# Kernel tuning notes

Measured on AMD Instinct MI355X. Metric: run time of the kernel, lower is better.

## Reference

```python
import jax, jax.numpy as jnp
import numpy as np

N_EMBD = 256; N_HEAD = 16; CTX = 2048
V_HD = 32; KV_RANK = 32; Q_RANK = 96
ROPE_HD = 64; NOPE_HD = 32; HEAD_D = ROPE_HD + NOPE_HD  # 96
N_KEEP = CTX // 4  # 512
C_CURV = 1.0
EPS = 1e-6
B, T = 2, 2048


def rmsnorm(x, w):
    return x * jax.lax.rsqrt(jnp.mean(x * x, axis=-1, keepdims=True) + EPS) * w


def logmap(x, u, c):
    # log map from hyperbolic point x toward u (Poincare ball, curvature c)
    xn = jnp.linalg.norm(x, axis=-1, keepdims=True)
    sf = 2.0 / (1.0 + c * xn ** 2)                      # scaling_factor(x, c)
    mx = -x
    un = jnp.linalg.norm(u, axis=-1, keepdims=True)
    ip = jnp.sum(mx * u, axis=-1, keepdims=True)
    num = (1 + 2 * c * ip + c * un ** 2) * mx + (1 - c * xn ** 2) * u
    den = 1 + 2 * c * ip + (c ** 2) * (xn ** 2) * (un ** 2)
    mob = num / den                                      # mobius_addition(-x, u, c)
    an = jnp.linalg.norm(mob, axis=-1, keepdims=True)
    cf = 2.0 / (sf * (c ** 0.5))
    arg = jnp.clip(jnp.sqrt(c) * jnp.sqrt(an), -0.999, 0.999)
    return cf * jnp.arctanh(arg) * (mob / an)


def rope_apply(x, cos_seq, sin_seq):
    # x: [B,H,T,D]; cos/sin: [T,D//2] -> broadcast [1,1,T,D//2]
    c = cos_seq[None, None]; s = sin_seq[None, None]
    xr, xi = jnp.split(x, 2, axis=-1)
    return jnp.concatenate([xr * c - xi * s, xr * s + xi * c], axis=-1)


def attn(q, k, v, causal):
    d = q.shape[-1]
    s = jnp.einsum('bhqd,bhkd->bhqk', q, k) / jnp.sqrt(jnp.asarray(d, q.dtype))
    if causal:
        mask = jnp.tril(jnp.ones((s.shape[-2], s.shape[-1]), bool))
        s = jnp.where(mask, s, -jnp.inf)
    p = jax.nn.softmax(s, axis=-1)
    return jnp.einsum('bhqk,bhkd->bhqd', p, v)


def setup_inputs() -> dict:
    key = jax.random.key(0)
    ks = jax.random.split(key, 20)
    w = lambda k, shp: (jax.random.normal(k, shp, jnp.float32) * 0.02)
    NOPE_DIM = N_HEAD * NOPE_HD   # 512
    ROPE_DIM = N_HEAD * ROPE_HD   # 1024
    VAL_DIM = N_HEAD * V_HD       # 512
    # precompute_freqs_cis(rope_head_dim, ctx_len)
    freqs = 1.0 / (10000.0 ** (np.arange(0, ROPE_HD, 2, dtype=np.float32) / ROPE_HD))
    t = np.arange(CTX, dtype=np.float32)
    ang = np.outer(t, freqs)
    return {
        'x': jax.random.normal(ks[0], (B, T, N_EMBD), jnp.float32),
        'W_cq': w(ks[1], (N_EMBD, Q_RANK)),
        'q_norm_w': jnp.ones((Q_RANK,), jnp.float32),
        'W_dqn': w(ks[2], (Q_RANK, NOPE_DIM)),
        'W_dqr': w(ks[3], (Q_RANK, ROPE_DIM)),
        'W_ckv': w(ks[4], (N_EMBD, KV_RANK)),
        'kv_norm_w': jnp.ones((KV_RANK,), jnp.float32),
        'W_dkn': w(ks[5], (KV_RANK, NOPE_DIM)),
        'W_dv': w(ks[6], (KV_RANK, VAL_DIM)),
        'W_kr': w(ks[7], (N_EMBD, ROPE_HD)),
        'W_imp': w(ks[8], (N_EMBD, 1)),
        'b_imp': jnp.zeros((1,), jnp.float32),
        'W_selk': w(ks[9], (N_EMBD, N_HEAD * HEAD_D)),
        'W_selv': w(ks[10], (N_EMBD, VAL_DIM)),
        'W_wink': w(ks[11], (N_EMBD, N_HEAD * HEAD_D)),
        'W_winv': w(ks[12], (N_EMBD, VAL_DIM)),
        'W_gate': w(ks[13], (N_EMBD, 3)),
        'b_gate': jnp.zeros((3,), jnp.float32),
        'W_proj': w(ks[14], (N_HEAD * V_HD, N_EMBD)),
        'cos_f': jnp.asarray(np.cos(ang)),
        'sin_f': jnp.asarray(np.sin(ang)),
    }


def reference(x, W_cq, q_norm_w, W_dqn, W_dqr, W_ckv, kv_norm_w, W_dkn, W_dv, W_kr,
              W_imp, b_imp, W_selk, W_selv, W_wink, W_winv, W_gate, b_gate, W_proj,
              cos_f, sin_f):
    Bx, Tx, C = x.shape
    ref = jnp.pad(x[:, :-1, :], ((0, 0), (1, 0), (0, 0)))   # calculate_reference_point
    xh = logmap(ref, x, C_CURV)
    # compressed query path
    nq = rmsnorm(xh @ W_cq, q_norm_w)
    qn = (nq @ W_dqn).reshape(Bx, Tx, N_HEAD, NOPE_HD).transpose(0, 2, 1, 3)
    qr = (nq @ W_dqr).reshape(Bx, Tx, N_HEAD, ROPE_HD).transpose(0, 2, 1, 3)
    qr = rope_apply(qr, cos_f[:Tx], sin_f[:Tx])
    q = jnp.concatenate([qn, qr], axis=-1)                  # [B,H,T,96]
    # branch gate
    bw = jax.nn.softmax(jnp.mean(x @ W_gate + b_gate, axis=1), axis=-1)  # [B,3]
    # compressed KV path
    nkv = rmsnorm(x @ W_ckv, kv_norm_w)
    kn = (nkv @ W_dkn).reshape(Bx, Tx, N_HEAD, NOPE_HD).transpose(0, 2, 1, 3)
    v = (nkv @ W_dv).reshape(Bx, Tx, N_HEAD, V_HD).transpose(0, 2, 1, 3)
    kr = rope_apply((x @ W_kr)[:, None], cos_f[:Tx], sin_f[:Tx])  # [B,1,T,64]
    kr = jnp.broadcast_to(kr, (Bx, N_HEAD, Tx, ROPE_HD))
    k = jnp.concatenate([kn, kr], axis=-1)
    out_cmp = attn(q, k, v, causal=True)
    # token-selection branch (top-k important tokens, sorted)
    scores = (x @ W_imp + b_imp)[..., 0]                    # [B,T]
    _, idx = jax.lax.top_k(scores, min(N_KEEP, Tx))
    idx = jnp.sort(idx, axis=1)
    sel = jnp.take_along_axis(x, idx[:, :, None], axis=1)   # [B,K,C]
    sk = (sel @ W_selk).reshape(Bx, -1, N_HEAD, HEAD_D).transpose(0, 2, 1, 3)
    sv = (sel @ W_selv).reshape(Bx, -1, N_HEAD, V_HD).transpose(0, 2, 1, 3)
    out_sel = attn(q, sk, sv, causal=False)
    # sliding-window branch (training path -> full sequence, causal)
    wk = (x @ W_wink).reshape(Bx, Tx, N_HEAD, HEAD_D).transpose(0, 2, 1, 3)
    wv = (x @ W_winv).reshape(Bx, Tx, N_HEAD, V_HD).transpose(0, 2, 1, 3)
    out_win = attn(q, wk, wv, causal=True)
    w3 = bw[:, :, None, None, None]
    out = w3[:, 0] * out_cmp + w3[:, 1] * out_sel + w3[:, 2] * out_win
    out = out.transpose(0, 2, 1, 3).reshape(Bx, Tx, N_HEAD * V_HD)
    return out @ W_proj
```

## Files before the change

### kernel.cpp

```cpp
#include <hip/hip_runtime.h>
#include <hip/hip_bf16.h>
#include <math.h>

#define TT 2048
#define NE 256
#define NHEAD 16

typedef __attribute__((ext_vector_type(8))) short bf16x8;
typedef __attribute__((ext_vector_type(4))) float f32x4;
typedef __attribute__((ext_vector_type(16))) float f32x16;
typedef unsigned short ushort;
typedef __attribute__((ext_vector_type(8))) unsigned short us8;

__device__ __forceinline__ short f2bf(float x) {
  __hip_bfloat16 h = __float2bfloat16(x);
  return *reinterpret_cast<short*>(&h);
}
__device__ __forceinline__ float bf2f(ushort u) {
  unsigned v = ((unsigned)u) << 16;
  return __uint_as_float(v);
}

__global__ __launch_bounds__(256) void logmap_kernel(const float* __restrict__ x,
                                                     ushort* __restrict__ xhb,
                                                     ushort* __restrict__ xbf) {
  __shared__ float red[16];
  int row = blockIdx.x, tid = threadIdx.x;
  int t = row & (TT - 1);
  float uv = x[row * NE + tid];
  float rv = (t == 0) ? 0.f : x[row * NE - NE + tid];
  xbf[row * NE + tid] = (ushort)f2bf(uv);
  float a = rv * rv, bq = uv * uv, c2 = -rv * uv;
#pragma unroll
  for (int off = 32; off > 0; off >>= 1) {
    a += __shfl_down(a, off, 64);
    bq += __shfl_down(bq, off, 64);
    c2 += __shfl_down(c2, off, 64);
  }
  if ((tid & 63) == 0) {
    int w = tid >> 6;
    red[w] = a; red[4 + w] = bq; red[8 + w] = c2;
  }
  __syncthreads();
  float xn2 = red[0] + red[1] + red[2] + red[3];
  float un2 = red[4] + red[5] + red[6] + red[7];
  float ip  = red[8] + red[9] + red[10] + red[11];
  float den = 1.f + 2.f * ip + xn2 * un2;
  float mob = ((1.f + 2.f * ip + un2) * (-rv) + (1.f - xn2) * uv) / den;
  float m2 = mob * mob;
#pragma unroll
  for (int off = 32; off > 0; off >>= 1) m2 += __shfl_down(m2, off, 64);
  if ((tid & 63) == 0) red[12 + (tid >> 6)] = m2;
  __syncthreads();
  float an2 = red[12] + red[13] + red[14] + red[15];
  float an = sqrtf(an2);
  float cf = 1.f + xn2;
  float arg = fminf(sqrtf(an), 0.999f);
  xhb[row * NE + tid] = (ushort)f2bf(cf * atanhf(arg) * mob / an);
}

__global__ __launch_bounds__(256) void wtconv_all_kernel(
    const float* __restrict__ W_dqn, const float* __restrict__ W_dqr,
    const float* __restrict__ W_dkn, const float* __restrict__ W_dv,
    const float* __restrict__ W_selk, const float* __restrict__ W_selv,
    const float* __restrict__ W_wink, const float* __restrict__ W_winv,
    const float* __restrict__ W_proj, const float* __restrict__ W_cq,
    const float* __restrict__ W_ckv, const float* __restrict__ W_kr,
    const float* __restrict__ W_gate, const float* __restrict__ W_imp,
    ushort* __restrict__ Wt_q, ushort* __restrict__ Wt_kv,
    ushort* __restrict__ Wt_sel, ushort* __restrict__ Wt_win,
    ushort* __restrict__ Wt_proj, ushort* __restrict__ Wt_cq,
    ushort* __restrict__ Wt_nkv) {
  int i = blockIdx.x * 256 + threadIdx.x;
  const float scale = 0.147244458176154f;
  if (i < 147456) {
    int k = i / 1536, n = i - k * 1536;
    float v = (n < 512) ? W_dqn[(size_t)k * 512 + n] : W_dqr[(size_t)k * 1024 + (n - 512)];
    Wt_q[(size_t)n * 96 + k] = (ushort)f2bf(v * scale);
  } else if (i < 180224) {
    int j = i - 147456;
    int k = j >> 10, n = j & 1023;
    float v = (n < 512) ? W_dkn[(size_t)k * 512 + n] : W_dv[(size_t)k * 512 + (n - 512)];
    Wt_kv[(size_t)n * 32 + k] = (ushort)f2bf(v);
  } else if (i < 704512) {
    int j = i - 180224;
    int k = j >> 11, n = j & 2047;
    float v = (n < 1536) ? W_selk[(size_t)k * 1536 + n] : W_selv[(size_t)k * 512 + (n - 1536)];
    Wt_sel[(size_t)n * 256 + k] = (ushort)f2bf(v);
  } else if (i < 1228800) {
    int j = i - 704512;
    int k = j >> 11, n = j & 2047;
    float v = (n < 1536) ? W_wink[(size_t)k * 1536 + n] : W_winv[(size_t)k * 512 + (n - 1536)];
    Wt_win[(size_t)n * 256 + k] = (ushort)f2bf(v);
  } else if (i < 1359872) {
    int j = i - 1228800;
    int k = j >> 8, n = j & 255;
    Wt_proj[(size_t)n * 512 + k] = (ushort)f2bf(W_proj[(size_t)k * 256 + n]);
  } else if (i < 1392640) {
    int j = i - 1359872;
    int k = j >> 7, n = j & 127;
    float v = (n < 96) ? W_cq[(size_t)k * 96 + n] : 0.f;
    Wt_cq[(size_t)n * 256 + k] = (ushort)f2bf(v);
  } else if (i < 1425408) {
    int j = i - 1392640;
    int k = j >> 7, n = j & 127;
    float v;
    if (n < 32) v = W_ckv[(size_t)k * 32 + n];
    else if (n < 96) v = W_kr[(size_t)k * 64 + (n - 32)];
    else if (n < 99) v = W_gate[(size_t)k * 3 + (n - 96)];
    else if (n == 99) v = W_imp[k];
    else v = 0.f;
    Wt_nkv[(size_t)n * 256 + k] = (ushort)f2bf(v);
  }
}

__global__ __launch_bounds__(256) void gemm_kernel(const ushort* __restrict__ A,
                                                   const ushort* __restrict__ Bt,
                                                   void* __restrict__ Out,
                                                   const ushort* __restrict__ A2,
                                                   const ushort* __restrict__ Bt2,
                                                   void* __restrict__ Out2,
                                                   const int* __restrict__ selidx,
                                                   const float* __restrict__ cosp,
                                                   const float* __restrict__ sinp,
                                                   int K, int ldo, int obf16, int ropemode) {
  __shared__ __align__(16) short As[128 * 40];
  __shared__ __align__(16) short Bs[128 * 40];
  if (blockIdx.z == 1) { A = A2; Bt = Bt2; Out = Out2; }
  int m0 = blockIdx.x * 128, n0 = blockIdx.y * 128;
  int tid = threadIdx.x;
  int wv = tid >> 6, lane = tid & 63;
  int l15 = lane & 15, quad = lane >> 4;
  int wm = wv >> 1, wn = wv & 1;

  int r = tid >> 1, seg = tid & 1;
  int arow = m0 + r;
  if (selidx) arow = ((arow >> 9) * TT) + selidx[m0 + r];
  const ushort* ga = A + (size_t)arow * K + seg * 16;
  const ushort* gb = Bt + (size_t)(n0 + r) * K + seg * 16;

  f32x4 acc[4][4];
#pragma unroll
  for (int i = 0; i < 4; ++i)
#pragma unroll
    for (int j = 0; j < 4; ++j) acc[i][j] = (f32x4){0.f, 0.f, 0.f, 0.f};

  int nk = K >> 5;
  us8 apre0 = *(const us8*)ga, apre1 = *(const us8*)(ga + 8);
  us8 bpre0 = *(const us8*)gb, bpre1 = *(const us8*)(gb + 8);
  for (int kk = 0; kk < nk; ++kk) {
    __syncthreads();
    *(us8*)(As + r * 40 + seg * 16) = apre0;
    *(us8*)(As + r * 40 + seg * 16 + 8) = apre1;
    *(us8*)(Bs + r * 40 + seg * 16) = bpre0;
    *(us8*)(Bs + r * 40 + seg * 16 + 8) = bpre1;
    __syncthreads();
    if (kk + 1 < nk) {
      apre0 = *(const us8*)(ga + (kk + 1) * 32);
      apre1 = *(const us8*)(ga + (kk + 1) * 32 + 8);
      bpre0 = *(const us8*)(gb + (kk + 1) * 32);
      bpre1 = *(const us8*)(gb + (kk + 1) * 32 + 8);
    }
    bf16x8 af[4], bf[4];
#pragma unroll
    for (int mf = 0; mf < 4; ++mf)
      af[mf] = *(const bf16x8*)(As + (wm * 64 + mf * 16 + l15) * 40 + quad * 8);
#pragma unroll
    for (int nf = 0; nf < 4; ++nf)
      bf[nf] = *(const bf16x8*)(Bs + (wn * 64 + nf * 16 + l15) * 40 + quad * 8);
#pragma unroll
    for (int mf = 0; mf < 4; ++mf)
#pragma unroll
      for (int nf = 0; nf < 4; ++nf)
        acc[mf][nf] = __builtin_amdgcn_mfma_f32_16x16x32_bf16(af[mf], bf[nf], acc[mf][nf], 0, 0, 0);
  }

  if (ropemode && blockIdx.y >= 4) {
#pragma unroll
    for (int mf = 0; mf < 4; ++mf) {
#pragma unroll
      for (int nf = 0; nf < 2; ++nf) {
        int dd = nf * 16 + l15;
#pragma unroll
        for (int reg = 0; reg < 4; ++reg) {
          int row = m0 + wm * 64 + mf * 16 + quad * 4 + reg;
          int t = row & (TT - 1);
          float c = cosp[t * 32 + dd], s = sinp[t * 32 + dd];
          float xr = acc[mf][nf][reg], xi = acc[mf][nf + 2][reg];
          int col = n0 + wn * 64 + nf * 16 + l15;
          size_t oi = (size_t)row * ldo + col;
          ((ushort*)Out)[oi] = (ushort)f2bf(xr * c - xi * s);
          ((ushort*)Out)[oi + 32] = (ushort)f2bf(xr * s + xi * c);
        }
      }
    }
    return;
  }
#pragma unroll
  for (int mf = 0; mf < 4; ++mf) {
#pragma unroll
    for (int nf = 0; nf < 4; ++nf) {
#pragma unroll
      for (int reg = 0; reg < 4; ++reg) {
        int row = m0 + wm * 64 + mf * 16 + quad * 4 + reg;
        int col = n0 + wn * 64 + nf * 16 + l15;
        size_t oi = (size_t)row * ldo + col;
        float v = acc[mf][nf][reg];
        if (obf16) ((ushort*)Out)[oi] = (ushort)f2bf(v);
        else ((float*)Out)[oi] = v;
      }
    }
  }
}

__global__ __launch_bounds__(128) void norm_kernel(const float* __restrict__ nkvraw,
                                                   const float* __restrict__ nqraw,
                                                   const float* __restrict__ x,
                                                   const float* __restrict__ W_imp,
                                                   const float* __restrict__ b_imp,
                                                   const float* __restrict__ kvnw,
                                                   const float* __restrict__ qnw,
                                                   const float* __restrict__ cos_t,
                                                   const float* __restrict__ sin_t,
                                                   ushort* __restrict__ nkvb,
                                                   ushort* __restrict__ krbf,
                                                   float* __restrict__ scores,
                                                   ushort* __restrict__ nqb) {
  int tid = threadIdx.x;
  if (blockIdx.x < 4096) {
    int row = blockIdx.x;
    int t = row & (TT - 1);
    if (tid < 32) {
      float v = nkvraw[(size_t)row * 128 + tid];
      float ss = v * v;
#pragma unroll
      for (int off = 16; off > 0; off >>= 1) ss += __shfl_xor(ss, off, 32);
      nkvb[(size_t)row * 32 + tid] = (ushort)f2bf(v * rsqrtf(ss / 32.f + 1e-6f) * kvnw[tid]);
    } else if (tid < 64) {
      int dd = tid - 32;
      float xr = nkvraw[(size_t)row * 128 + 32 + dd];
      float xi = nkvraw[(size_t)row * 128 + 64 + dd];
      float c = cos_t[t * 32 + dd], s = sin_t[t * 32 + dd];
      krbf[(size_t)row * 64 + dd] = (ushort)f2bf(xr * c - xi * s);
      krbf[(size_t)row * 64 + dd + 32] = (ushort)f2bf(xr * s + xi * c);
    } else {
      int lane = tid - 64;
      float p = 0.f;
#pragma unroll
      for (int k = 0; k < 4; ++k) p += x[(size_t)row * 256 + lane + k * 64] * W_imp[lane + k * 64];
#pragma unroll
      for (int off = 32; off > 0; off >>= 1) p += __shfl_down(p, off, 64);
      if (lane == 0) scores[row] = p + b_imp[0];
    }
  } else {
    int row = blockIdx.x - 4096;
    __shared__ float red2[2];
    float v = (tid < 96) ? nqraw[(size_t)row * 128 + tid] : 0.f;
    float p = v * v;
#pragma unroll
    for (int off = 32; off > 0; off >>= 1) p += __shfl_down(p, off, 64);
    if ((tid & 63) == 0) red2[tid >> 6] = p;
    __syncthreads();
    float ss = red2[0] + red2[1];
    float sc = rsqrtf(ss / 96.f + 1e-6f);
    if (tid < 96) nqb[(size_t)row * 96 + tid] = (ushort)f2bf(v * sc * qnw[tid]);
  }
}

__global__ __launch_bounds__(256) void gate_kernel(const float* __restrict__ nkvraw,
                                                   const float* __restrict__ b_gate,
                                                   float* __restrict__ bw) {
  int tid = threadIdx.x;
  float a0 = 0, a1 = 0, a2 = 0, a3 = 0, a4 = 0, a5 = 0;
  for (int r = tid; r < 2 * TT; r += 256) {
    float g0 = nkvraw[(size_t)r * 128 + 96];
    float g1 = nkvraw[(size_t)r * 128 + 97];
    float g2 = nkvraw[(size_t)r * 128 + 98];
    if (r < TT) { a0 += g0; a1 += g1; a2 += g2; }
    else { a3 += g0; a4 += g1; a5 += g2; }
  }
  __shared__ float red[6][256];
  red[0][tid] = a0; red[1][tid] = a1; red[2][tid] = a2;
  red[3][tid] = a3; red[4][tid] = a4; red[5][tid] = a5;
  __syncthreads();
  for (int s = 128; s > 0; s >>= 1) {
    if (tid < s) {
#pragma unroll
      for (int q = 0; q < 6; ++q) red[q][tid] += red[q][tid + s];
    }
    __syncthreads();
  }
  if (tid == 0) {
    for (int b = 0; b < 2; ++b) {
      float v[3];
      float mx = -INFINITY;
      for (int j = 0; j < 3; ++j) {
        v[j] = red[b * 3 + j][0] / (float)TT + b_gate[j];
        mx = fmaxf(mx, v[j]);
      }
      float sum = 0.f;
      for (int j = 0; j < 3; ++j) { v[j] = expf(v[j] - mx); sum += v[j]; }
      for (int j = 0; j < 3; ++j) bw[b * 3 + j] = v[j] / sum;
    }
  }
}

__global__ __launch_bounds__(1024) void topk_rank_kernel(const float* __restrict__ scores,
                                                         int* __restrict__ flags) {
  int b = blockIdx.y, blk = blockIdx.x;
  int tid = threadIdx.x;
  __shared__ unsigned sk[TT];
#pragma unroll
  for (int e = 0; e < 2; ++e) {
    int i = tid + e * 1024;
    float s = scores[b * TT + i];
    unsigned u = __float_as_uint(s);
    u = (u & 0x80000000u) ? ~u : (u | 0x80000000u);
    sk[i] = u;
  }
  __syncthreads();
  int e = blk * 64 + (tid >> 4);
  int sub = tid & 15;
  unsigned u = sk[e];
  int r = 0;
  int j0 = sub * 128;
#pragma unroll 8
  for (int j = j0; j < j0 + 128; ++j) {
    unsigned v = sk[j];
    r += (int)((v > u) || (v == u && j < e));
  }
#pragma unroll
  for (int off = 8; off > 0; off >>= 1) r += __shfl_down(r, off, 16);
  if (sub == 0) flags[b * TT + e] = (r < 512) ? 1 : 0;
}

__global__ __launch_bounds__(1024) void topk_scan_kernel(const int* __restrict__ flags,
                                                         int* __restrict__ selidx) {
  int b = blockIdx.x, tid = threadIdx.x;
  __shared__ int pre[TT];
  int f0 = flags[b * TT + tid], f1 = flags[b * TT + tid + 1024];
  pre[tid] = f0;
  pre[tid + 1024] = f1;
  __syncthreads();
  for (int off = 1; off < TT; off <<= 1) {
    int a0 = (tid >= off) ? pre[tid - off] : 0;
    int a1 = (tid + 1024 >= off) ? pre[tid + 1024 - off] : 0;
    __syncthreads();
    pre[tid] += a0;
    pre[tid + 1024] += a1;
    __syncthreads();
  }
  if (f0) selidx[b * 512 + pre[tid] - 1] = tid;
  if (f1) selidx[b * 512 + pre[tid + 1024] - 1] = tid + 1024;
}

__global__ __launch_bounds__(256, 2) void flash_fused_kernel(
    const ushort* __restrict__ qbf,
    const ushort* __restrict__ kv,
    const ushort* __restrict__ krbf,
    const ushort* __restrict__ selt,
    const ushort* __restrict__ wint,
    const float* __restrict__ bw,
    ushort* __restrict__ attout) {
  __shared__ __align__(16) short Qs[128 * 104];
  __shared__ __align__(16) short Ks[2][64 * 104];
  __shared__ __align__(16) short Vts[2][32 * 72];
  __shared__ float Ls[4][32];

  int bx = blockIdx.x;
  int j = bx >> 5;
  int qtile = (j < 8) ? (15 - 2 * j) : (2 * (j - 8));
  int bh = bx & 31;
  int b = bh >> 4, h = bh & 15;
  int tid = threadIdx.x;
  int wv = tid >> 6, lane = tid & 63;
  int l31 = lane & 31, half = lane >> 5;

  int qrow0 = qtile * 128;
  for (int i = tid; i < 128 * 24; i += 256) {
    int qi = i / 24, dp = (i - qi * 24) * 4;
    int col = (dp < 32) ? (h * 32 + dp) : (512 + h * 64 + (dp - 32));
    *(ushort4*)(Qs + qi * 104 + dp) =
        *(const ushort4*)(qbf + (size_t)(b * TT + qrow0 + qi) * 1536 + col);
  }
  __syncthreads();
  bf16x8 qf[6];
#pragma unroll
  for (int ks = 0; ks < 6; ++ks)
    qf[ks] = *(const bf16x8*)(Qs + (wv * 32 + l31) * 104 + ks * 16 + half * 8);

  short* kdst[6];
#pragma unroll
  for (int c = 0; c < 6; ++c) {
    int i = c * 256 + tid;
    int kj = i / 24, dp = (i - kj * 24) * 4;
    kdst[c] = &Ks[0][kj * 104 + dp];
  }
  short* vdsta[2];
  short* vdstb[2];
#pragma unroll
  for (int c = 0; c < 2; ++c) {
    int i = c * 256 + tid;
    int d0 = (i & 15) * 2, kjp = (i >> 4) * 2;
    vdsta[c] = &Vts[0][(d0 + 0) * 72 + kjp];
    vdstb[c] = &Vts[0][(d0 + 1) * 72 + kjp];
  }

  f32x16 oacc;
#pragma unroll
  for (int r = 0; r < 16; ++r) oacc[r] = 0.f;

  for (int s = 0; s < 3; ++s) {
    const ushort *kb1, *kb2, *vb;
    size_t krs1, krs2, vrs;
    int split, Tk, causal;
    if (s == 0) {
      kb1 = kv + h * 32;        krs1 = 1024; split = 32;
      kb2 = krbf;               krs2 = 64;
      vb = kv + 512 + h * 32;   vrs = 1024;
      Tk = TT; causal = 1;
    } else if (s == 1) {
      kb1 = selt + h * 96;      krs1 = 2048; split = 96;
      kb2 = selt;               krs2 = 2048;
      vb = selt + 1536 + h * 32; vrs = 2048;
      Tk = 512; causal = 0;
    } else {
      kb1 = wint + h * 96;      krs1 = 2048; split = 96;
      kb2 = wint;               krs2 = 2048;
      vb = wint + 1536 + h * 32; vrs = 2048;
      Tk = TT; causal = 1;
    }
    size_t bTk = (size_t)b * Tk;

    const ushort* ksrc[6];
    int kstep[6];
#pragma unroll
    for (int c = 0; c < 6; ++c) {
      int i = c * 256 + tid;
      int kj = i / 24, dp = (i - kj * 24) * 4;
      if (dp < split) { ksrc[c] = kb1 + (bTk + kj) * krs1 + dp; kstep[c] = (int)(64 * krs1); }
      else            { ksrc[c] = kb2 + (bTk + kj) * krs2 + (dp - split); kstep[c] = (int)(64 * krs2); }
    }
    const ushort* vsrcA[2];
    const ushort* vsrcB[2];
    int vstep = (int)(64 * vrs);
#pragma unroll
    for (int c = 0; c < 2; ++c) {
      int i = c * 256 + tid;
      int d0 = (i & 15) * 2, kjp = (i >> 4) * 2;
      vsrcA[c] = vb + (bTk + kjp) * vrs + d0;
      vsrcB[c] = vb + (bTk + kjp + 1) * vrs + d0;
    }

    ushort4 kpre0[6], kpre1[6];
    ushort2 vpa0[2], vpb0[2], vpa1[2], vpb1[2];

#define PREFETCH(KP, VA, VB)                                  \
  {                                                           \
    _Pragma("unroll") for (int c = 0; c < 6; ++c) {           \
      KP[c] = *(const ushort4*)ksrc[c];                       \
      ksrc[c] += kstep[c];                                    \
    }                                                         \
    _Pragma("unroll") for (int c = 0; c < 2; ++c) {           \
      VA[c] = *(const ushort2*)vsrcA[c];                      \
      VB[c] = *(const ushort2*)vsrcB[c];                      \
      vsrcA[c] += vstep;                                      \
      vsrcB[c] += vstep;                                      \
    }                                                         \
  }

#define COMMIT(KP, VA, VB, SL)                                           \
  {                                                                      \
    _Pragma("unroll") for (int c = 0; c < 6; ++c)                        \
      *(ushort4*)(kdst[c] + (SL) * (64 * 104)) = KP[c];                  \
    _Pragma("unroll") for (int c = 0; c < 2; ++c) {                      \
      *(unsigned*)(vdsta[c] + (SL) * (32 * 72)) =                        \
          (unsigned)VA[c].x | ((unsigned)VB[c].x << 16);                 \
      *(unsigned*)(vdstb[c] + (SL) * (32 * 72)) =                        \
          (unsigned)VA[c].y | ((unsigned)VB[c].y << 16);                 \
    }                                                                    \
  }

    f32x16 of;
#pragma unroll
    for (int r = 0; r < 16; ++r) of[r] = 0.f;
    float lsum = 0.f;

    auto do_tile = [&](int kt, const short* Kss, const short* Vss) {
      int krow0 = kt * 64;
      f32x16 sfT[2];
#pragma unroll
      for (int r = 0; r < 16; ++r) { sfT[0][r] = 0.f; sfT[1][r] = 0.f; }
#pragma unroll
      for (int ks = 0; ks < 6; ++ks) {
#pragma unroll
        for (int kb = 0; kb < 2; ++kb) {
          bf16x8 ak = *(const bf16x8*)(Kss + (kb * 32 + l31) * 104 + ks * 16 + half * 8);
          sfT[kb] = __builtin_amdgcn_mfma_f32_32x32x16_bf16(ak, qf[ks], sfT[kb], 0, 0, 0);
        }
      }
      int qg = qrow0 + wv * 32 + l31;
      int domask = causal && (kt >= 2 * qtile);
      unsigned w01[2][4], w23[2][4];
#pragma unroll
      for (int kb = 0; kb < 2; ++kb) {
#pragma unroll
        for (int g = 0; g < 4; ++g) {
          int key0 = krow0 + kb * 32 + 8 * g + 4 * half;
          float s0 = sfT[kb][g * 4 + 0];
          float s1 = sfT[kb][g * 4 + 1];
          float s2 = sfT[kb][g * 4 + 2];
          float s3 = sfT[kb][g * 4 + 3];
          if (domask) {
            if (key0 + 0 > qg) s0 = -INFINITY;
            if (key0 + 1 > qg) s1 = -INFINITY;
            if (key0 + 2 > qg) s2 = -INFINITY;
            if (key0 + 3 > qg) s3 = -INFINITY;
          }
          float p0 = __builtin_amdgcn_exp2f(fminf(s0, 43.3f));
          float p1 = __builtin_amdgcn_exp2f(fminf(s1, 43.3f));
          float p2 = __builtin_amdgcn_exp2f(fminf(s2, 43.3f));
          float p3 = __builtin_amdgcn_exp2f(fminf(s3, 43.3f));
          lsum += (p0 + p1) + (p2 + p3);
          asm("v_cvt_pk_bf16_f32 %0, %1, %2" : "=v"(w01[kb][g]) : "v"(p0), "v"(p1));
          asm("v_cvt_pk_bf16_f32 %0, %1, %2" : "=v"(w23[kb][g]) : "v"(p2), "v"(p3));
        }
      }
#pragma unroll
      for (int ks2 = 0; ks2 < 4; ++ks2) {
        int kb = ks2 >> 1, gA = 2 * (ks2 & 1);
        unsigned a0 = w01[kb][gA], b0 = w01[kb][gA + 1];
        unsigned a1 = w23[kb][gA], b1 = w23[kb][gA + 1];
        asm("v_permlane32_swap_b32 %0, %1" : "+v"(a0), "+v"(b0));
        asm("v_permlane32_swap_b32 %0, %1" : "+v"(a1), "+v"(b1));
        union { unsigned u[4]; bf16x8 v; } ap;
        ap.u[0] = a0; ap.u[1] = a1; ap.u[2] = b0; ap.u[3] = b1;
        bf16x8 bv = *(const bf16x8*)(Vss + l31 * 72 + ks2 * 16 + half * 8);
        of = __builtin_amdgcn_mfma_f32_32x32x16_bf16(ap.v, bv, of, 0, 0, 0);
      }
    };

    int nkt = causal ? (2 * qtile + 2) : 8;
    PREFETCH(kpre0, vpa0, vpb0);
    PREFETCH(kpre1, vpa1, vpb1);
    for (int kt = 0; kt < nkt; kt += 2) {
      COMMIT(kpre0, vpa0, vpb0, 0);
      if (kt + 2 < nkt) PREFETCH(kpre0, vpa0, vpb0);
      __syncthreads();
      do_tile(kt, Ks[0], Vts[0]);
      COMMIT(kpre1, vpa1, vpb1, 1);
      if (kt + 3 < nkt) PREFETCH(kpre1, vpa1, vpb1);
      __syncthreads();
      do_tile(kt + 1, Ks[1], Vts[1]);
    }
#undef PREFETCH
#undef COMMIT

    lsum += __shfl_xor(lsum, 32, 64);
    if (half == 0) Ls[wv][l31] = lsum;
    asm volatile("s_waitcnt lgkmcnt(0)" ::: "memory");
    float wgt = bw[b * 3 + s];
#pragma unroll
    for (int reg = 0; reg < 16; ++reg) {
      int ql = (reg & 3) + 8 * (reg >> 2) + 4 * half;
      oacc[reg] += of[reg] * (wgt / Ls[wv][ql]);
    }
  }

#pragma unroll
  for (int reg = 0; reg < 16; ++reg) {
    int trow = qrow0 + wv * 32 + (reg & 3) + 8 * (reg >> 2) + 4 * half;
    attout[(size_t)(b * TT + trow) * 512 + h * 32 + l31] = (ushort)f2bf(oacc[reg]);
  }
}

extern "C" void kernel_launch(void* const* d_in, const int* in_sizes, int n_in,
                              void* d_out, int out_size, void* d_ws, size_t ws_size,
                              hipStream_t stream) {
  const float* x      = (const float*)d_in[0];
  const float* W_cq   = (const float*)d_in[1];
  const float* qnw    = (const float*)d_in[2];
  const float* W_dqn  = (const float*)d_in[3];
  const float* W_dqr  = (const float*)d_in[4];
  const float* W_ckv  = (const float*)d_in[5];
  const float* kvnw   = (const float*)d_in[6];
  const float* W_dkn  = (const float*)d_in[7];
  const float* W_dv   = (const float*)d_in[8];
  const float* W_kr   = (const float*)d_in[9];
  const float* W_imp  = (const float*)d_in[10];
  const float* b_imp  = (const float*)d_in[11];
  const float* W_selk = (const float*)d_in[12];
  const float* W_selv = (const float*)d_in[13];
  const float* W_wink = (const float*)d_in[14];
  const float* W_winv = (const float*)d_in[15];
  const float* W_gate = (const float*)d_in[16];
  const float* b_gate = (const float*)d_in[17];
  const float* W_proj = (const float*)d_in[18];
  const float* cos_f  = (const float*)d_in[19];
  const float* sin_f  = (const float*)d_in[20];
  float* out = (float*)d_out;
  float* ws  = (float*)d_ws;

  size_t off = 0;
  auto alloc = [&](size_t n) {
    float* p = ws + off;
    off += (n + 255) & ~(size_t)255;
    return p;
  };
  const int ROWS = 2 * TT;
  ushort* xbf     = (ushort*)alloc((size_t)ROWS * 128);
  ushort* xhb     = (ushort*)alloc((size_t)ROWS * 128);
  float* nqraw    = alloc((size_t)ROWS * 128);
  float* nkvraw   = alloc((size_t)ROWS * 128);
  ushort* nqb     = (ushort*)alloc((size_t)ROWS * 48);
  ushort* qbf     = (ushort*)alloc((size_t)ROWS * 768);
  ushort* nkvb    = (ushort*)alloc((size_t)ROWS * 16);
  ushort* kvtmp   = (ushort*)alloc((size_t)ROWS * 512);
  ushort* krbf    = (ushort*)alloc((size_t)ROWS * 32);
  float* scores   = alloc(ROWS);
  float* bwp      = alloc(8);
  int* selidx     = (int*)alloc(1024);
  int* selflags   = (int*)alloc(ROWS);
  ushort* seltmp  = (ushort*)alloc((size_t)1024 * 1024);
  ushort* wintmp  = (ushort*)alloc((size_t)ROWS * 1024);
  ushort* attoutb = (ushort*)alloc((size_t)ROWS * 256);
  ushort* Wt_q    = (ushort*)alloc((size_t)1536 * 48);
  ushort* Wt_kv   = (ushort*)alloc((size_t)1024 * 16);
  ushort* Wt_sel  = (ushort*)alloc((size_t)2048 * 128);
  ushort* Wt_win  = (ushort*)alloc((size_t)2048 * 128);
  ushort* Wt_proj = (ushort*)alloc((size_t)256 * 256);
  ushort* Wt_cq   = (ushort*)alloc((size_t)128 * 128);
  ushort* Wt_nkv  = (ushort*)alloc((size_t)128 * 128);

  wtconv_all_kernel<<<5568, 256, 0, stream>>>(
      W_dqn, W_dqr, W_dkn, W_dv, W_selk, W_selv, W_wink, W_winv, W_proj,
      W_cq, W_ckv, W_kr, W_gate, W_imp,
      Wt_q, Wt_kv, Wt_sel, Wt_win, Wt_proj, Wt_cq, Wt_nkv);

  logmap_kernel<<<ROWS, 256, 0, stream>>>(x, xhb, xbf);

  gemm_kernel<<<dim3(32, 1, 2), 256, 0, stream>>>(xhb, Wt_cq, nqraw, xbf, Wt_nkv, nkvraw,
                                                  nullptr, nullptr, nullptr, 256, 128, 0, 0);
  norm_kernel<<<2 * ROWS, 128, 0, stream>>>(nkvraw, nqraw, x, W_imp, b_imp, kvnw, qnw,
                                            cos_f, sin_f, nkvb, krbf, scores, nqb);
  gemm_kernel<<<dim3(32, 12), 256, 0, stream>>>(nqb, Wt_q, qbf, nullptr, nullptr, nullptr,
                                                nullptr, cos_f, sin_f, 96, 1536, 1, 1);
  gemm_kernel<<<dim3(32, 8), 256, 0, stream>>>(nkvb, Wt_kv, kvtmp, nullptr, nullptr, nullptr,
                                               nullptr, nullptr, nullptr, 32, 1024, 1, 0);
  gate_kernel<<<1, 256, 0, stream>>>(nkvraw, b_gate, bwp);
  topk_rank_kernel<<<dim3(32, 2), 1024, 0, stream>>>(scores, selflags);
  topk_scan_kernel<<<2, 1024, 0, stream>>>(selflags, selidx);
  gemm_kernel<<<dim3(8, 16), 256, 0, stream>>>(xbf, Wt_sel, seltmp, nullptr, nullptr, nullptr,
                                               selidx, nullptr, nullptr, 256, 2048, 1, 0);
  gemm_kernel<<<dim3(32, 16), 256, 0, stream>>>(xbf, Wt_win, wintmp, nullptr, nullptr, nullptr,
                                                nullptr, nullptr, nullptr, 256, 2048, 1, 0);

  flash_fused_kernel<<<512, 256, 0, stream>>>(qbf, kvtmp, krbf, seltmp, wintmp, bwp, attoutb);

  gemm_kernel<<<dim3(32, 2), 256, 0, stream>>>(attoutb, Wt_proj, out, nullptr, nullptr, nullptr,
                                               nullptr, nullptr, nullptr, 512, 256, 0, 0);
}
```

Before: 294.0 us.

## Split fused attention branches across blocks and combine partial outputs in a separate pass

The three attention branches (compressed, selected, window) now run in separate blocks instead of sequentially inside one block, tripling the grid to 1536 blocks. Each block writes its weighted fp32 partial output to a scratch buffer, and a new combine kernel sums the three partials into bf16. Shared memory is compacted by reusing the Q staging area for the K tiles, and launch bounds request 4 blocks per CU. This targets low occupancy and long serial per-block work, at the cost of extra fp32 global traffic, a second kernel launch, and reloading Q three times.

```diff
diff --git a/kernel.cpp b/kernel.cpp
--- a/kernel.cpp
+++ b/kernel.cpp
@@ -354,23 +354,25 @@
   if (f1) selidx[b * 512 + pre[tid + 1024] - 1] = tid + 1024;
 }
 
-__global__ __launch_bounds__(256, 2) void flash_fused_kernel(
+__global__ __launch_bounds__(256, 4) void flash_fused_kernel(
     const ushort* __restrict__ qbf,
     const ushort* __restrict__ kv,
     const ushort* __restrict__ krbf,
     const ushort* __restrict__ selt,
     const ushort* __restrict__ wint,
     const float* __restrict__ bw,
-    ushort* __restrict__ attout) {
-  __shared__ __align__(16) short Qs[128 * 104];
-  __shared__ __align__(16) short Ks[2][64 * 104];
-  __shared__ __align__(16) short Vts[2][32 * 72];
-  __shared__ float Ls[4][32];
+    float* __restrict__ attp) {
+  __shared__ __align__(16) short smem[13312 + 4608 + 256];
+  short* Ksm = smem;
+  short* Vtm = smem + 13312;
+  float* Ls  = (float*)(smem + 17920);
 
   int bx = blockIdx.x;
-  int j = bx >> 5;
+  int s = bx % 3;
+  int r = bx / 3;
+  int j = r >> 5;
   int qtile = (j < 8) ? (15 - 2 * j) : (2 * (j - 8));
-  int bh = bx & 31;
+  int bh = r & 31;
   int b = bh >> 4, h = bh & 15;
   int tid = threadIdx.x;
   int wv = tid >> 6, lane = tid & 63;
@@ -380,21 +382,43 @@
   for (int i = tid; i < 128 * 24; i += 256) {
     int qi = i / 24, dp = (i - qi * 24) * 4;
     int col = (dp < 32) ? (h * 32 + dp) : (512 + h * 64 + (dp - 32));
-    *(ushort4*)(Qs + qi * 104 + dp) =
+    *(ushort4*)(Ksm + qi * 104 + dp) =
         *(const ushort4*)(qbf + (size_t)(b * TT + qrow0 + qi) * 1536 + col);
   }
   __syncthreads();
   bf16x8 qf[6];
 #pragma unroll
   for (int ks = 0; ks < 6; ++ks)
-    qf[ks] = *(const bf16x8*)(Qs + (wv * 32 + l31) * 104 + ks * 16 + half * 8);
+    qf[ks] = *(const bf16x8*)(Ksm + (wv * 32 + l31) * 104 + ks * 16 + half * 8);
+  __syncthreads();
+
+  const ushort *kb1, *kb2, *vb;
+  size_t krs1, krs2, vrs;
+  int split, Tk, causal;
+  if (s == 0) {
+    kb1 = kv + h * 32;        krs1 = 1024; split = 32;
+    kb2 = krbf;               krs2 = 64;
+    vb = kv + 512 + h * 32;   vrs = 1024;
+    Tk = TT; causal = 1;
+  } else if (s == 1) {
+    kb1 = selt + h * 96;      krs1 = 2048; split = 96;
+    kb2 = selt;               krs2 = 2048;
+    vb = selt + 1536 + h * 32; vrs = 2048;
+    Tk = 512; causal = 0;
+  } else {
+    kb1 = wint + h * 96;      krs1 = 2048; split = 96;
+    kb2 = wint;               krs2 = 2048;
+    vb = wint + 1536 + h * 32; vrs = 2048;
+    Tk = TT; causal = 1;
+  }
+  size_t bTk = (size_t)b * Tk;
 
   short* kdst[6];
 #pragma unroll
   for (int c = 0; c < 6; ++c) {
     int i = c * 256 + tid;
     int kj = i / 24, dp = (i - kj * 24) * 4;
-    kdst[c] = &Ks[0][kj * 104 + dp];
+    kdst[c] = &Ksm[kj * 104 + dp];
   }
   short* vdsta[2];
   short* vdstb[2];
@@ -402,58 +426,31 @@
   for (int c = 0; c < 2; ++c) {
     int i = c * 256 + tid;
     int d0 = (i & 15) * 2, kjp = (i >> 4) * 2;
-    vdsta[c] = &Vts[0][(d0 + 0) * 72 + kjp];
-    vdstb[c] = &Vts[0][(d0 + 1) * 72 + kjp];
-  }
-
-  f32x16 oacc;
-#pragma unroll
-  for (int r = 0; r < 16; ++r) oacc[r] = 0.f;
-
-  for (int s = 0; s < 3; ++s) {
-    const ushort *kb1, *kb2, *vb;
-    size_t krs1, krs2, vrs;
-    int split, Tk, causal;
-    if (s == 0) {
-      kb1 = kv + h * 32;        krs1 = 1024; split = 32;
-      kb2 = krbf;               krs2 = 64;
-      vb = kv + 512 + h * 32;   vrs = 1024;
-      Tk = TT; causal = 1;
-    } else if (s == 1) {
-      kb1 = selt + h * 96;      krs1 = 2048; split = 96;
-      kb2 = selt;               krs2 = 2048;
-      vb = selt + 1536 + h * 32; vrs = 2048;
-      Tk = 512; causal = 0;
-    } else {
-      kb1 = wint + h * 96;      krs1 = 2048; split = 96;
-      kb2 = wint;               krs2 = 2048;
-      vb = wint + 1536 + h * 32; vrs = 2048;
-      Tk = TT; causal = 1;
-    }
-    size_t bTk = (size_t)b * Tk;
-
-    const ushort* ksrc[6];
-    int kstep[6];
-#pragma unroll
-    for (int c = 0; c < 6; ++c) {
-      int i = c * 256 + tid;
-      int kj = i / 24, dp = (i - kj * 24) * 4;
-      if (dp < split) { ksrc[c] = kb1 + (bTk + kj) * krs1 + dp; kstep[c] = (int)(64 * krs1); }
-      else            { ksrc[c] = kb2 + (bTk + kj) * krs2 + (dp - split); kstep[c] = (int)(64 * krs2); }
-    }
-    const ushort* vsrcA[2];
-    const ushort* vsrcB[2];
-    int vstep = (int)(64 * vrs);
-#pragma unroll
-    for (int c = 0; c < 2; ++c) {
-      int i = c * 256 + tid;
-      int d0 = (i & 15) * 2, kjp = (i >> 4) * 2;
-      vsrcA[c] = vb + (bTk + kjp) * vrs + d0;
-      vsrcB[c] = vb + (bTk + kjp + 1) * vrs + d0;
-    }
-
-    ushort4 kpre0[6], kpre1[6];
-    ushort2 vpa0[2], vpb0[2], vpa1[2], vpb1[2];
+    vdsta[c] = &Vtm[(d0 + 0) * 72 + kjp];
+    vdstb[c] = &Vtm[(d0 + 1) * 72 + kjp];
+  }
+  const ushort* ksrc[6];
+  int kstep[6];
+#pragma unroll
+  for (int c = 0; c < 6; ++c) {
+    int i = c * 256 + tid;
+    int kj = i / 24, dp = (i - kj * 24) * 4;
+    if (dp < split) { ksrc[c] = kb1 + (bTk + kj) * krs1 + dp; kstep[c] = (int)(64 * krs1); }
+    else            { ksrc[c] = kb2 + (bTk + kj) * krs2 + (dp - split); kstep[c] = (int)(64 * krs2); }
+  }
+  const ushort* vsrcA[2];
+  const ushort* vsrcB[2];
+  int vstep = (int)(64 * vrs);
+#pragma unroll
+  for (int c = 0; c < 2; ++c) {
+    int i = c * 256 + tid;
+    int d0 = (i & 15) * 2, kjp = (i >> 4) * 2;
+    vsrcA[c] = vb + (bTk + kjp) * vrs + d0;
+    vsrcB[c] = vb + (bTk + kjp + 1) * vrs + d0;
+  }
+
+  ushort4 kpre0[6], kpre1[6];
+  ushort2 vpa0[2], vpb0[2], vpa1[2], vpb1[2];
 
 #define PREFETCH(KP, VA, VB)                                  \
   {                                                           \
@@ -481,97 +478,107 @@
     }                                                                    \
   }
 
-    f32x16 of;
-#pragma unroll
-    for (int r = 0; r < 16; ++r) of[r] = 0.f;
-    float lsum = 0.f;
-
-    auto do_tile = [&](int kt, const short* Kss, const short* Vss) {
-      int krow0 = kt * 64;
-      f32x16 sfT[2];
-#pragma unroll
-      for (int r = 0; r < 16; ++r) { sfT[0][r] = 0.f; sfT[1][r] = 0.f; }
-#pragma unroll
-      for (int ks = 0; ks < 6; ++ks) {
-#pragma unroll
-        for (int kb = 0; kb < 2; ++kb) {
-          bf16x8 ak = *(const bf16x8*)(Kss + (kb * 32 + l31) * 104 + ks * 16 + half * 8);
-          sfT[kb] = __builtin_amdgcn_mfma_f32_32x32x16_bf16(ak, qf[ks], sfT[kb], 0, 0, 0);
+  f32x16 of;
+#pragma unroll
+  for (int r2 = 0; r2 < 16; ++r2) of[r2] = 0.f;
+  float lsum = 0.f;
+
+  auto do_tile = [&](int kt, const short* Kss, const short* Vss) {
+    int krow0 = kt * 64;
+    f32x16 sfT[2];
+#pragma unroll
+    for (int r2 = 0; r2 < 16; ++r2) { sfT[0][r2] = 0.f; sfT[1][r2] = 0.f; }
+#pragma unroll
+    for (int ks = 0; ks < 6; ++ks) {
+#pragma unroll
+      for (int kb = 0; kb < 2; ++kb) {
+        bf16x8 ak = *(const bf16x8*)(Kss + (kb * 32 + l31) * 104 + ks * 16 + half * 8);
+        sfT[kb] = __builtin_amdgcn_mfma_f32_32x32x16_bf16(ak, qf[ks], sfT[kb], 0, 0, 0);
+      }
+    }
+    int qg = qrow0 + wv * 32 + l31;
+    int domask = causal && (kt >= 2 * qtile);
+    unsigned w01[2][4], w23[2][4];
+#pragma unroll
+    for (int kb = 0; kb < 2; ++kb) {
+#pragma unroll
+      for (int g = 0; g < 4; ++g) {
+        int key0 = krow0 + kb * 32 + 8 * g + 4 * half;
+        float s0 = sfT[kb][g * 4 + 0];
+        float s1 = sfT[kb][g * 4 + 1];
+        float s2 = sfT[kb][g * 4 + 2];
+        float s3 = sfT[kb][g * 4 + 3];
+        if (domask) {
+          if (key0 + 0 > qg) s0 = -INFINITY;
+          if (key0 + 1 > qg) s1 = -INFINITY;
+          if (key0 + 2 > qg) s2 = -INFINITY;
+          if (key0 + 3 > qg) s3 = -INFINITY;
         }
+        float p0 = __builtin_amdgcn_exp2f(fminf(s0, 43.3f));
+        float p1 = __builtin_amdgcn_exp2f(fminf(s1, 43.3f));
+        float p2 = __builtin_amdgcn_exp2f(fminf(s2, 43.3f));
+        float p3 = __builtin_amdgcn_exp2f(fminf(s3, 43.3f));
+        lsum += (p0 + p1) + (p2 + p3);
+        asm("v_cvt_pk_bf16_f32 %0, %1, %2" : "=v"(w01[kb][g]) : "v"(p0), "v"(p1));
+        asm("v_cvt_pk_bf16_f32 %0, %1, %2" : "=v"(w23[kb][g]) : "v"(p2), "v"(p3));
       }
-      int qg = qrow0 + wv * 32 + l31;
-      int domask = causal && (kt >= 2 * qtile);
-      unsigned w01[2][4], w23[2][4];
-#pragma unroll
-      for (int kb = 0; kb < 2; ++kb) {
-#pragma unroll
-        for (int g = 0; g < 4; ++g) {
-          int key0 = krow0 + kb * 32 + 8 * g + 4 * half;
-          float s0 = sfT[kb][g * 4 + 0];
-          float s1 = sfT[kb][g * 4 + 1];
-          float s2 = sfT[kb][g * 4 + 2];
-          float s3 = sfT[kb][g * 4 + 3];
-          if (domask) {
-            if (key0 + 0 > qg) s0 = -INFINITY;
-            if (key0 + 1 > qg) s1 = -INFINITY;
-            if (key0 + 2 > qg) s2 = -INFINITY;
-            if (key0 + 3 > qg) s3 = -INFINITY;
-          }
-          float p0 = __builtin_amdgcn_exp2f(fminf(s0, 43.3f));
-          float p1 = __builtin_amdgcn_exp2f(fminf(s1, 43.3f));
-          float p2 = __builtin_amdgcn_exp2f(fminf(s2, 43.3f));
-          float p3 = __builtin_amdgcn_exp2f(fminf(s3, 43.3f));
-          lsum += (p0 + p1) + (p2 + p3);
-          asm("v_cvt_pk_bf16_f32 %0, %1, %2" : "=v"(w01[kb][g]) : "v"(p0), "v"(p1));
-          asm("v_cvt_pk_bf16_f32 %0, %1, %2" : "=v"(w23[kb][g]) : "v"(p2), "v"(p3));
-        }
-      }
-#pragma unroll
-      for (int ks2 = 0; ks2 < 4; ++ks2) {
-        int kb = ks2 >> 1, gA = 2 * (ks2 & 1);
-        unsigned a0 = w01[kb][gA], b0 = w01[kb][gA + 1];
-        unsigned a1 = w23[kb][gA], b1 = w23[kb][gA + 1];
-        asm("v_permlane32_swap_b32 %0, %1" : "+v"(a0), "+v"(b0));
-        asm("v_permlane32_swap_b32 %0, %1" : "+v"(a1), "+v"(b1));
-        union { unsigned u[4]; bf16x8 v; } ap;
-        ap.u[0] = a0; ap.u[1] = a1; ap.u[2] = b0; ap.u[3] = b1;
-        bf16x8 bv = *(const bf16x8*)(Vss + l31 * 72 + ks2 * 16 + half * 8);
-        of = __builtin_amdgcn_mfma_f32_32x32x16_bf16(ap.v, bv, of, 0, 0, 0);
-      }
-    };
-
-    int nkt = causal ? (2 * qtile + 2) : 8;
-    PREFETCH(kpre0, vpa0, vpb0);
-    PREFETCH(kpre1, vpa1, vpb1);
-    for (int kt = 0; kt < nkt; kt += 2) {
-      COMMIT(kpre0, vpa0, vpb0, 0);
-      if (kt + 2 < nkt) PREFETCH(kpre0, vpa0, vpb0);
-      __syncthreads();
-      do_tile(kt, Ks[0], Vts[0]);
-      COMMIT(kpre1, vpa1, vpb1, 1);
-      if (kt + 3 < nkt) PREFETCH(kpre1, vpa1, vpb1);
-      __syncthreads();
-      do_tile(kt + 1, Ks[1], Vts[1]);
-    }
+    }
+#pragma unroll
+    for (int ks2 = 0; ks2 < 4; ++ks2) {
+      int kb = ks2 >> 1, gA = 2 * (ks2 & 1);
+      unsigned a0 = w01[kb][gA], b0 = w01[kb][gA + 1];
+      unsigned a1 = w23[kb][gA], b1 = w23[kb][gA + 1];
+      asm("v_permlane32_swap_b32 %0, %1" : "+v"(a0), "+v"(b0));
+      asm("v_permlane32_swap_b32 %0, %1" : "+v"(a1), "+v"(b1));
+      union { unsigned u[4]; bf16x8 v; } ap;
+      ap.u[0] = a0; ap.u[1] = a1; ap.u[2] = b0; ap.u[3] = b1;
+      bf16x8 bv = *(const bf16x8*)(Vss + l31 * 72 + ks2 * 16 + half * 8);
+      of = __builtin_amdgcn_mfma_f32_32x32x16_bf16(ap.v, bv, of, 0, 0, 0);
+    }
+  };
+
+  int nkt = causal ? (2 * qtile + 2) : 8;
+  PREFETCH(kpre0, vpa0, vpb0);
+  PREFETCH(kpre1, vpa1, vpb1);
+  for (int kt = 0; kt < nkt; kt += 2) {
+    COMMIT(kpre0, vpa0, vpb0, 0);
+    if (kt + 2 < nkt) PREFETCH(kpre0, vpa0, vpb0);
+    __syncthreads();
+    do_tile(kt, Ksm, Vtm);
+    COMMIT(kpre1, vpa1, vpb1, 1);
+    if (kt + 3 < nkt) PREFETCH(kpre1, vpa1, vpb1);
+    __syncthreads();
+    do_tile(kt + 1, Ksm + 64 * 104, Vtm + 32 * 72);
+  }
 #undef PREFETCH
 #undef COMMIT
 
-    lsum += __shfl_xor(lsum, 32, 64);
-    if (half == 0) Ls[wv][l31] = lsum;
-    asm volatile("s_waitcnt lgkmcnt(0)" ::: "memory");
-    float wgt = bw[b * 3 + s];
-#pragma unroll
-    for (int reg = 0; reg < 16; ++reg) {
-      int ql = (reg & 3) + 8 * (reg >> 2) + 4 * half;
-      oacc[reg] += of[reg] * (wgt / Ls[wv][ql]);
-    }
-  }
-
+  lsum += __shfl_xor(lsum, 32, 64);
+  if (half == 0) Ls[wv * 32 + l31] = lsum;
+  asm volatile("s_waitcnt lgkmcnt(0)" ::: "memory");
+  float wgt = bw[b * 3 + s];
+  float* op = attp + (size_t)s * (4096 * 512);
 #pragma unroll
   for (int reg = 0; reg < 16; ++reg) {
-    int trow = qrow0 + wv * 32 + (reg & 3) + 8 * (reg >> 2) + 4 * half;
-    attout[(size_t)(b * TT + trow) * 512 + h * 32 + l31] = (ushort)f2bf(oacc[reg]);
-  }
+    int ql = (reg & 3) + 8 * (reg >> 2) + 4 * half;
+    int trow = qrow0 + wv * 32 + ql;
+    op[(size_t)(b * TT + trow) * 512 + h * 32 + l31] = of[reg] * (wgt / Ls[wv * 32 + ql]);
+  }
+}
+
+__global__ __launch_bounds__(256) void att_combine_kernel(const float* __restrict__ attp,
+                                                          ushort* __restrict__ attout) {
+  int i = blockIdx.x * 256 + threadIdx.x;
+  const f32x4* p = (const f32x4*)attp;
+  f32x4 a = p[i];
+  f32x4 c1 = p[i + 524288];
+  f32x4 c2 = p[i + 1048576];
+  ushort4 o;
+  o.x = (ushort)f2bf(a[0] + c1[0] + c2[0]);
+  o.y = (ushort)f2bf(a[1] + c1[1] + c2[1]);
+  o.z = (ushort)f2bf(a[2] + c1[2] + c2[2]);
+  o.w = (ushort)f2bf(a[3] + c1[3] + c2[3]);
+  *(ushort4*)(attout + (size_t)i * 4) = o;
 }
 
 extern "C" void kernel_launch(void* const* d_in, const int* in_sizes, int n_in,
@@ -624,6 +631,7 @@
   ushort* seltmp  = (ushort*)alloc((size_t)1024 * 1024);
   ushort* wintmp  = (ushort*)alloc((size_t)ROWS * 1024);
   ushort* attoutb = (ushort*)alloc((size_t)ROWS * 256);
+  float* attp     = alloc((size_t)3 * ROWS * 512);
   ushort* Wt_q    = (ushort*)alloc((size_t)1536 * 48);
   ushort* Wt_kv   = (ushort*)alloc((size_t)1024 * 16);
   ushort* Wt_sel  = (ushort*)alloc((size_t)2048 * 128);
@@ -655,7 +663,8 @@
   gemm_kernel<<<dim3(32, 16), 256, 0, stream>>>(xbf, Wt_win, wintmp, nullptr, nullptr, nullptr,
                                                 nullptr, nullptr, nullptr, 256, 2048, 1, 0);
 
-  flash_fused_kernel<<<512, 256, 0, stream>>>(qbf, kvtmp, krbf, seltmp, wintmp, bwp, attoutb);
+  flash_fused_kernel<<<1536, 256, 0, stream>>>(qbf, kvtmp, krbf, seltmp, wintmp, bwp, attp);
+  att_combine_kernel<<<2048, 256, 0, stream>>>(attp, attoutb);
 
   gemm_kernel<<<dim3(32, 2), 256, 0, stream>>>(attoutb, Wt_proj, out, nullptr, nullptr, nullptr,
                                                nullptr, nullptr, nullptr, 512, 256, 0, 0);
```

Measured after the change: 590.8 us. 101% more time.
